# Kernel tuning notes

Measured on AMD Instinct MI355X. Metric: run time of the kernel, lower is better.

Reference implementation:

```python
import jax, jax.numpy as jnp
import numpy as np

TOP_K = 2
NUM_EXPERTS = 8
CAPACITY_FACTOR = 1.0


def setup_inputs() -> dict:
    key = jax.random.key(0)
    k1, k2, k3, k4 = jax.random.split(key, 4)
    sl, bs, hs, ffn = 2048, 2, 1024, 4096
    x = jax.random.normal(k1, (sl, bs, hs), dtype=jnp.float32)
    router_w = jax.random.normal(k2, (hs, NUM_EXPERTS), dtype=jnp.float32) * 0.02
    w1 = jax.random.normal(k3, (NUM_EXPERTS, hs, ffn), dtype=jnp.float32) * 0.02
    w2 = jax.random.normal(k4, (NUM_EXPERTS, ffn, hs), dtype=jnp.float32) * 0.02
    bias = jnp.zeros((1, 1, hs), dtype=jnp.float32)
    return {"x": x, "router_w": router_w, "w1": w1, "w2": w2, "bias": bias}


def _moe_forward(x, router_w, w1, w2):
    sl, bs, hs = x.shape
    xf = x.reshape(-1, hs)                                   # [T, H]
    T = xf.shape[0]
    TK = T * TOP_K
    capacity = int(CAPACITY_FACTOR * TOP_K * T / NUM_EXPERTS)  # static

    # Router: softmax over experts, then top-k (LearnedRouter)
    scores = jax.nn.softmax(xf @ router_w, axis=-1)          # [T, E]
    expert_weights, top_experts = jax.lax.top_k(scores, TOP_K)  # [T, K]
    ew = expert_weights.reshape(-1)                          # [T*K]
    te = top_experts.reshape(-1).astype(jnp.int32)           # [T*K]

    # indices_and_bins: stable sort by expert id + histogram + inclusive cumsum
    indices = jnp.argsort(te, stable=True)                   # sorted pos -> flat slot
    tokens_per_expert = jnp.zeros((NUM_EXPERTS,), jnp.int32).at[te].add(1)
    bins = jnp.cumsum(tokens_per_expert)                     # inclusive cumsum
    starts = bins - tokens_per_expert                        # exclusive offsets

    # binned_gather -> [E, capacity, H]; tokens beyond capacity are dropped
    c_range = jnp.arange(capacity)
    pos = starts[:, None] + c_range[None, :]                 # [E, C] positions in sorted order
    valid = c_range[None, :] < tokens_per_expert[:, None]    # [E, C]
    slot = indices[jnp.clip(pos, 0, TK - 1)]                 # flat (token*K + k) slot
    tok = slot // TOP_K                                      # source token row
    gathered = jnp.where(valid[..., None], xf[tok], 0.0)     # [E, C, H]

    # grouped expert MLP: gelu(x @ w1) @ w2  (megablocks mlp.MLP)
    h = jax.nn.gelu(jnp.einsum('ech,ehf->ecf', gathered, w1))
    y = jnp.einsum('ecf,efh->ech', h, w2)                    # [E, C, H]

    # binned_scatter: weighted accumulate back to token rows
    p = jnp.arange(TK)
    e_of_p = jnp.searchsorted(bins, p, side='right')         # expert of sorted pos
    c_of_p = p - starts[e_of_p]                              # slot within expert bin
    ok = c_of_p < capacity                                   # dropped tokens contribute 0
    vals = jnp.where(ok[:, None], y[e_of_p, jnp.clip(c_of_p, 0, capacity - 1)], 0.0)
    flat = indices                                           # flat slot at sorted pos p
    w = ew[flat]
    out = jnp.zeros((T, hs), x.dtype).at[flat // TOP_K].add(w[:, None] * vals)
    return out.reshape(sl, bs, hs)


def reference(x, router_w, w1, w2, bias):
    out = _moe_forward(x, router_w, w1, w2)
    return (out, bias)
```

## Files before the change

kernel.cpp:

```cpp
#include <hip/hip_runtime.h>
#include <hip/hip_bf16.h>


#define T_TOK 4096
#define HS 1024
#define FFN 4096
#define NE 8
#define CAP 1024
#define TKS 8192

#define WS_TE   67108864
#define WS_EW   67141632
#define WS_PERM 67174400
#define WS_WT   67239936
#define WS_XB   134348800

typedef float f4 __attribute__((ext_vector_type(4)));
typedef __bf16 bf16x8 __attribute__((ext_vector_type(8)));
typedef float f32x4 __attribute__((ext_vector_type(4)));

__device__ __forceinline__ void gld_lds16(const void* g, void* l) {
    __builtin_amdgcn_global_load_lds(
        (const __attribute__((address_space(1))) unsigned int*)g,
        (__attribute__((address_space(3))) unsigned int*)l, 16, 0, 0);
}

__global__ void init_out_kernel(float* __restrict__ out, const float* __restrict__ bias) {
    int i = blockIdx.x * 256 + threadIdx.x;
    const int TH = T_TOK * HS;
    if (i < TH) out[i] = 0.0f;
    else if (i < TH + HS) out[i] = bias[i - TH];
}

__global__ __launch_bounds__(256) void router_kernel(const float* __restrict__ x,
                                                     const float* __restrict__ rw,
                                                     int* __restrict__ te,
                                                     float* __restrict__ ew,
                                                     __bf16* __restrict__ xb) {
    __shared__ float rwt[NE * HS];
    int tid = threadIdx.x;
    for (int i = tid; i < NE * HS; i += 256) {
        int h = i >> 3, e = i & 7;
        rwt[e * HS + h] = rw[i];
    }
    __syncthreads();
    int wave = tid >> 6, lane = tid & 63;
    int t = blockIdx.x * 4 + wave;
    const float* xr = x + (size_t)t * HS;
    float s[NE];
    float xv[16];
#pragma unroll
    for (int e = 0; e < NE; ++e) s[e] = 0.0f;
#pragma unroll
    for (int j = 0; j < 16; ++j) {
        int h = lane + j * 64;
        xv[j] = xr[h];
#pragma unroll
        for (int e = 0; e < NE; ++e) s[e] += xv[j] * rwt[e * HS + h];
    }
#pragma unroll
    for (int j = 0; j < 16; ++j)
        xb[(size_t)t * HS + lane + j * 64] = (__bf16)xv[j];
#pragma unroll
    for (int e = 0; e < NE; ++e) {
#pragma unroll
        for (int off = 1; off < 64; off <<= 1) s[e] += __shfl_xor(s[e], off, 64);
    }
    float m = s[0];
#pragma unroll
    for (int e = 1; e < NE; ++e) m = fmaxf(m, s[e]);
    float psum = 0.0f;
#pragma unroll
    for (int e = 0; e < NE; ++e) psum += __expf(s[e] - m);
    int e0 = 0; float v0 = s[0];
#pragma unroll
    for (int e = 1; e < NE; ++e) { if (s[e] > v0) { v0 = s[e]; e0 = e; } }
    int e1 = -1; float v1 = -1e30f;
#pragma unroll
    for (int e = 0; e < NE; ++e) { if (e != e0 && s[e] > v1) { v1 = s[e]; e1 = e; } }
    if (lane == 0) {
        float inv = 1.0f / psum;
        te[2 * t]     = e0;
        te[2 * t + 1] = e1;
        ew[2 * t]     = __expf(v0 - m) * inv;
        ew[2 * t + 1] = __expf(v1 - m) * inv;
    }
}

__global__ __launch_bounds__(256) void sort_kernel(const int* __restrict__ te,
                                                   int* __restrict__ perm) {
    __shared__ int hist[256 * NE];
    int tid = threadIdx.x;
#pragma unroll
    for (int e = 0; e < NE; ++e) hist[tid * NE + e] = 0;
    for (int i = tid; i < TKS; i += 256) perm[i] = -1;
    __syncthreads();
    for (int j = 0; j < 32; ++j) {
        int p = tid * 32 + j;
        hist[tid * NE + te[p]]++;
    }
    __syncthreads();
    if (tid < NE) {
        int run = 0;
        for (int i = 0; i < 256; ++i) {
            int v = hist[i * NE + tid];
            hist[i * NE + tid] = run;
            run += v;
        }
    }
    __syncthreads();
    for (int j = 0; j < 32; ++j) {
        int p = tid * 32 + j;
        int e = te[p];
        int c = hist[tid * NE + e]++;
        if (c < CAP) perm[e * CAP + c] = p;
    }
}

__global__ __launch_bounds__(256) void conv_wt_kernel(const float* __restrict__ w,
                                                      __bf16* __restrict__ wt,
                                                      int K, int N) {
    __shared__ __bf16 t[64][72];
    const int e = blockIdx.z;
    const int kb = blockIdx.y * 64, nb = blockIdx.x * 64;
    const int tid = threadIdx.x;
    const float* src = w + ((size_t)e * K + kb) * N + nb;
    {
        const int kk = tid >> 4, nc = (tid & 15) * 4;
#pragma unroll
        for (int i = 0; i < 4; ++i) {
            int k = kk + 16 * i;
            f4 v = *(const f4*)(src + (size_t)k * N + nc);
            t[nc + 0][k] = (__bf16)v[0];
            t[nc + 1][k] = (__bf16)v[1];
            t[nc + 2][k] = (__bf16)v[2];
            t[nc + 3][k] = (__bf16)v[3];
        }
    }
    __syncthreads();
    __bf16* dst = wt + ((size_t)e * N + nb) * K + kb;
    const int nn = tid >> 3, ch = (tid & 7) * 8;
#pragma unroll
    for (int i = 0; i < 2; ++i) {
        int n = nn + 32 * i;
        bf16x8 v = *(const bf16x8*)(&t[n][ch]);
        *(bf16x8*)(dst + (size_t)n * K + ch) = v;
    }
}


#define STAGE8(c_, koff_) do {                                              \
    _Pragma("unroll")                                                       \
    for (int j = 0; j < 4; ++j) {                                           \
        gld_lds16(aptr[j] + (koff_), &As[c_][j * 32 + w * 8][0]);           \
        gld_lds16(bptr[j] + (koff_), &Bs[c_][j * 32 + w * 8][0]);           \
    }                                                                       \
} while (0)

#define TILE_BODY(c_) do {                                                  \
    _Pragma("unroll")                                                       \
    for (int kk = 0; kk < 2; ++kk) {                                        \
        const int g = (kk * 4 + (lane >> 4)) ^ (lane & 7);                  \
        bf16x8 af[4], bb[4];                                                \
        _Pragma("unroll")                                                   \
        for (int mi = 0; mi < 4; ++mi)                                      \
            af[mi] = *(const bf16x8*)&As[c_][wr * 64 + mi * 16 + l15][g * 8]; \
        _Pragma("unroll")                                                   \
        for (int ni = 0; ni < 4; ++ni)                                      \
            bb[ni] = *(const bf16x8*)&Bs[c_][wc * 64 + ni * 16 + l15][g * 8]; \
        __builtin_amdgcn_s_setprio(1);                                      \
        _Pragma("unroll")                                                   \
        for (int mi = 0; mi < 4; ++mi)                                      \
            _Pragma("unroll")                                               \
            for (int ni = 0; ni < 4; ++ni)                                  \
                acc[mi][ni] = __builtin_amdgcn_mfma_f32_16x16x32_bf16(      \
                    af[mi], bb[ni], acc[mi][ni], 0, 0, 0);                  \
        __builtin_amdgcn_s_setprio(0);                                      \
    }                                                                       \
} while (0)

#define KTILE_SYNC() do {                                                   \
    asm volatile("s_waitcnt vmcnt(0)" ::: "memory");                        \
    __builtin_amdgcn_s_barrier();                                           \
    asm volatile("" ::: "memory");                                          \
} while (0)

__global__ __launch_bounds__(256, 2) void gemm1_kernel(const __bf16* __restrict__ xb,
                                                       const __bf16* __restrict__ w1t,
                                                       const int* __restrict__ perm,
                                                       __bf16* __restrict__ hbuf) {
    __shared__ __bf16 As[2][128][64];
    __shared__ __bf16 Bs[2][128][64];
    const int e = blockIdx.z, mblk = blockIdx.y, nblk = blockIdx.x;
    const int tid = threadIdx.x, lane = tid & 63, w = tid >> 6;
    const int wr = w >> 1, wc = w & 1;
    const int l15 = lane & 15;
    const int srl = lane >> 3;
    const int gsrc = (lane & 7) ^ srl;

    const __bf16* aptr[4];
    const __bf16* bptr[4];
#pragma unroll
    for (int j = 0; j < 4; ++j) {
        int arow = j * 32 + w * 8 + srl;
        int p = perm[e * CAP + mblk * 128 + arow];
        int tok = (p < 0) ? 0 : (p >> 1);
        aptr[j] = xb + (size_t)tok * HS + gsrc * 8;
        int brow = nblk * 128 + j * 32 + w * 8 + srl;
        bptr[j] = w1t + ((size_t)e * FFN + brow) * HS + gsrc * 8;
    }

    f32x4 acc[4][4];
#pragma unroll
    for (int mi = 0; mi < 4; ++mi)
#pragma unroll
        for (int ni = 0; ni < 4; ++ni) acc[mi][ni] = (f32x4)0.0f;

    const int NT = HS / 64;
    STAGE8(0, 0);
    KTILE_SYNC();
    int c = 0;
    for (int t = 0; t < NT; ++t) {
        if (t + 1 < NT) STAGE8(c ^ 1, (t + 1) * 64);
        TILE_BODY(c);
        KTILE_SYNC();
        c ^= 1;
    }

    const int mbase = mblk * 128 + wr * 64;
    const int nbase = nblk * 128 + wc * 64;
#pragma unroll
    for (int mi = 0; mi < 4; ++mi) {
#pragma unroll
        for (int ni = 0; ni < 4; ++ni) {
#pragma unroll
            for (int reg = 0; reg < 4; ++reg) {
                int mrow = mbase + mi * 16 + (lane >> 4) * 4 + reg;
                int ncol = nbase + ni * 16 + l15;
                float z = acc[mi][ni][reg];
                float u = 0.7978845608028654f * (z + 0.044715f * z * z * z);
                float tt = 1.0f - 2.0f / (1.0f + __expf(2.0f * u));
                float gv = 0.5f * z * (1.0f + tt);
                hbuf[(size_t)(e * CAP + mrow) * FFN + ncol] = (__bf16)gv;
            }
        }
    }
}

__global__ __launch_bounds__(256, 2) void gemm2_kernel(const __bf16* __restrict__ hbuf,
                                                       const __bf16* __restrict__ w2t,
                                                       const int* __restrict__ perm,
                                                       const float* __restrict__ ew,
                                                       float* __restrict__ out) {
    __shared__ __bf16 As[2][128][64];
    __shared__ __bf16 Bs[2][128][64];
    const int e = blockIdx.z;
    const int mblk = blockIdx.y, nblk = blockIdx.x;
    const int tid = threadIdx.x, lane = tid & 63, w = tid >> 6;
    const int wr = w >> 1, wc = w & 1;
    const int l15 = lane & 15;
    const int srl = lane >> 3;
    const int gsrc = (lane & 7) ^ srl;

    const __bf16* aptr[4];
    const __bf16* bptr[4];
#pragma unroll
    for (int j = 0; j < 4; ++j) {
        int arow = j * 32 + w * 8 + srl;
        aptr[j] = hbuf + ((size_t)(e * CAP + mblk * 128 + arow)) * FFN + gsrc * 8;
        int brow = nblk * 128 + j * 32 + w * 8 + srl;
        bptr[j] = w2t + ((size_t)e * HS + brow) * FFN + gsrc * 8;
    }

    f32x4 acc[4][4];
#pragma unroll
    for (int mi = 0; mi < 4; ++mi)
#pragma unroll
        for (int ni = 0; ni < 4; ++ni) acc[mi][ni] = (f32x4)0.0f;

    const int NT = FFN / 64;
    STAGE8(0, 0);
    KTILE_SYNC();
    int c = 0;
    for (int t = 0; t < NT; ++t) {
        if (t + 1 < NT) STAGE8(c ^ 1, (t + 1) * 64);
        TILE_BODY(c);
        KTILE_SYNC();
        c ^= 1;
    }

    int* sperm = (int*)&As[0][0][0];
    float* swt = (float*)(sperm + 128);
    if (tid < 128) {
        int p = perm[e * CAP + mblk * 128 + tid];
        sperm[tid] = p;
        swt[tid] = (p >= 0) ? ew[p] : 0.0f;
    }
    __syncthreads();

    const int nbase = nblk * 128 + wc * 64;
#pragma unroll
    for (int mi = 0; mi < 4; ++mi) {
#pragma unroll
        for (int reg = 0; reg < 4; ++reg) {
            int mloc = wr * 64 + mi * 16 + (lane >> 4) * 4 + reg;
            int p = sperm[mloc];
            if (p >= 0) {
                int tok = p >> 1;
                float wgt = swt[mloc];
#pragma unroll
                for (int ni = 0; ni < 4; ++ni) {
                    int n = nbase + ni * 16 + l15;
                    atomicAdd(&out[(size_t)tok * HS + n], wgt * acc[mi][ni][reg]);
                }
            }
        }
    }
}

extern "C" void kernel_launch(void* const* d_in, const int* in_sizes, int n_in,
                              void* d_out, int out_size, void* d_ws, size_t ws_size,
                              hipStream_t stream) {
    const float* x    = (const float*)d_in[0];
    const float* rw   = (const float*)d_in[1];
    const float* w1   = (const float*)d_in[2];
    const float* w2   = (const float*)d_in[3];
    const float* bias = (const float*)d_in[4];
    float* out = (float*)d_out;
    char* ws = (char*)d_ws;

    __bf16* hbuf = (__bf16*)ws;
    int*    te   = (int*)(ws + WS_TE);
    float*  ew   = (float*)(ws + WS_EW);
    int*    perm = (int*)(ws + WS_PERM);
    __bf16* wt   = (__bf16*)(ws + WS_WT);
    __bf16* xb   = (__bf16*)(ws + WS_XB);

    hipLaunchKernelGGL(init_out_kernel, dim3((T_TOK * HS + HS + 255) / 256), dim3(256),
                       0, stream, out, bias);
    hipLaunchKernelGGL(router_kernel, dim3(T_TOK / 4), dim3(256), 0, stream,
                       x, rw, te, ew, xb);
    hipLaunchKernelGGL(sort_kernel, dim3(1), dim3(256), 0, stream, te, perm);
    hipLaunchKernelGGL(conv_wt_kernel, dim3(FFN / 64, HS / 64, NE), dim3(256),
                       0, stream, w1, wt, HS, FFN);
    hipLaunchKernelGGL(gemm1_kernel, dim3(FFN / 128, CAP / 128, NE), dim3(256),
                       0, stream, xb, wt, perm, hbuf);
    hipLaunchKernelGGL(conv_wt_kernel, dim3(HS / 64, FFN / 64, NE), dim3(256),
                       0, stream, w2, wt, FFN, HS);
    hipLaunchKernelGGL(gemm2_kernel, dim3(HS / 128, CAP / 128, NE), dim3(256),
                       0, stream, hbuf, wt, perm, ew, out);
}
```

Before: 300.6 us.

## Single-buffer GEMM K-loop, remap blocks for XCD locality, cheaper GELU epilogue

Both expert GEMMs drop LDS double buffering and use a simple load-wait-sync-compute-sync loop with half the shared memory. The occupancy hint is removed from launch bounds. The 3D grid becomes a 1D grid whose block index is remapped so consecutive blocks of the same expert and M-block land on the same XCD, which is meant to improve L2 reuse of weights and activations. The tanh-GELU epilogue is rewritten in the equivalent sigmoid form with a fast reciprocal. The cost is that global loads no longer overlap with MFMA work inside a block.

After: 281.4 us. 1.07x faster.

```diff
diff --git a/kernel.cpp b/kernel.cpp
--- a/kernel.cpp
+++ b/kernel.cpp
@@ -149,25 +149,25 @@
 }
 
 
-#define STAGE8(c_, koff_) do {                                              \
+#define STAGE8(koff_) do {                                                  \
     _Pragma("unroll")                                                       \
     for (int j = 0; j < 4; ++j) {                                           \
-        gld_lds16(aptr[j] + (koff_), &As[c_][j * 32 + w * 8][0]);           \
-        gld_lds16(bptr[j] + (koff_), &Bs[c_][j * 32 + w * 8][0]);           \
+        gld_lds16(aptr[j] + (koff_), &As[j * 32 + w * 8][0]);               \
+        gld_lds16(bptr[j] + (koff_), &Bs[j * 32 + w * 8][0]);               \
     }                                                                       \
 } while (0)
 
-#define TILE_BODY(c_) do {                                                  \
+#define TILE_BODY() do {                                                    \
     _Pragma("unroll")                                                       \
     for (int kk = 0; kk < 2; ++kk) {                                        \
         const int g = (kk * 4 + (lane >> 4)) ^ (lane & 7);                  \
         bf16x8 af[4], bb[4];                                                \
         _Pragma("unroll")                                                   \
         for (int mi = 0; mi < 4; ++mi)                                      \
-            af[mi] = *(const bf16x8*)&As[c_][wr * 64 + mi * 16 + l15][g * 8]; \
+            af[mi] = *(const bf16x8*)&As[wr * 64 + mi * 16 + l15][g * 8];   \
         _Pragma("unroll")                                                   \
         for (int ni = 0; ni < 4; ++ni)                                      \
-            bb[ni] = *(const bf16x8*)&Bs[c_][wc * 64 + ni * 16 + l15][g * 8]; \
+            bb[ni] = *(const bf16x8*)&Bs[wc * 64 + ni * 16 + l15][g * 8];   \
         __builtin_amdgcn_s_setprio(1);                                      \
         _Pragma("unroll")                                                   \
         for (int mi = 0; mi < 4; ++mi)                                      \
@@ -179,19 +179,27 @@
     }                                                                       \
 } while (0)
 
-#define KTILE_SYNC() do {                                                   \
-    asm volatile("s_waitcnt vmcnt(0)" ::: "memory");                        \
-    __builtin_amdgcn_s_barrier();                                           \
-    asm volatile("" ::: "memory");                                          \
+#define KLOOP(NT_) do {                                                     \
+    for (int t = 0; t < (NT_); ++t) {                                       \
+        STAGE8(t * 64);                                                     \
+        asm volatile("s_waitcnt vmcnt(0)" ::: "memory");                    \
+        __syncthreads();                                                    \
+        TILE_BODY();                                                        \
+        __syncthreads();                                                    \
+    }                                                                       \
 } while (0)
 
-__global__ __launch_bounds__(256, 2) void gemm1_kernel(const __bf16* __restrict__ xb,
-                                                       const __bf16* __restrict__ w1t,
-                                                       const int* __restrict__ perm,
-                                                       __bf16* __restrict__ hbuf) {
-    __shared__ __bf16 As[2][128][64];
-    __shared__ __bf16 Bs[2][128][64];
-    const int e = blockIdx.z, mblk = blockIdx.y, nblk = blockIdx.x;
+__global__ __launch_bounds__(256) void gemm1_kernel(const __bf16* __restrict__ xb,
+                                                    const __bf16* __restrict__ w1t,
+                                                    const int* __restrict__ perm,
+                                                    __bf16* __restrict__ hbuf) {
+    __shared__ __bf16 As[128][64];
+    __shared__ __bf16 Bs[128][64];
+    const int hw = blockIdx.x;
+    const int logical = (hw & 7) * 256 + (hw >> 3);
+    const int nblk = logical & 31;
+    const int mblk = (logical >> 5) & 7;
+    const int e    = logical >> 8;
     const int tid = threadIdx.x, lane = tid & 63, w = tid >> 6;
     const int wr = w >> 1, wc = w & 1;
     const int l15 = lane & 15;
@@ -216,16 +224,7 @@
 #pragma unroll
         for (int ni = 0; ni < 4; ++ni) acc[mi][ni] = (f32x4)0.0f;
 
-    const int NT = HS / 64;
-    STAGE8(0, 0);
-    KTILE_SYNC();
-    int c = 0;
-    for (int t = 0; t < NT; ++t) {
-        if (t + 1 < NT) STAGE8(c ^ 1, (t + 1) * 64);
-        TILE_BODY(c);
-        KTILE_SYNC();
-        c ^= 1;
-    }
+    KLOOP(HS / 64);
 
     const int mbase = mblk * 128 + wr * 64;
     const int nbase = nblk * 128 + wc * 64;
@@ -238,24 +237,28 @@
                 int mrow = mbase + mi * 16 + (lane >> 4) * 4 + reg;
                 int ncol = nbase + ni * 16 + l15;
                 float z = acc[mi][ni][reg];
-                float u = 0.7978845608028654f * (z + 0.044715f * z * z * z);
-                float tt = 1.0f - 2.0f / (1.0f + __expf(2.0f * u));
-                float gv = 0.5f * z * (1.0f + tt);
+                float z2 = z * z;
+                float y = z * (1.5957691216057308f + 0.07135481627f * z2);
+                float ex = __expf(-y);
+                float gv = z * __builtin_amdgcn_rcpf(1.0f + ex);
                 hbuf[(size_t)(e * CAP + mrow) * FFN + ncol] = (__bf16)gv;
             }
         }
     }
 }
 
-__global__ __launch_bounds__(256, 2) void gemm2_kernel(const __bf16* __restrict__ hbuf,
-                                                       const __bf16* __restrict__ w2t,
-                                                       const int* __restrict__ perm,
-                                                       const float* __restrict__ ew,
-                                                       float* __restrict__ out) {
-    __shared__ __bf16 As[2][128][64];
-    __shared__ __bf16 Bs[2][128][64];
-    const int e = blockIdx.z;
-    const int mblk = blockIdx.y, nblk = blockIdx.x;
+__global__ __launch_bounds__(256) void gemm2_kernel(const __bf16* __restrict__ hbuf,
+                                                    const __bf16* __restrict__ w2t,
+                                                    const int* __restrict__ perm,
+                                                    const float* __restrict__ ew,
+                                                    float* __restrict__ out) {
+    __shared__ __bf16 As[128][64];
+    __shared__ __bf16 Bs[128][64];
+    const int hw = blockIdx.x;
+    const int logical = (hw & 7) * 64 + (hw >> 3);
+    const int nblk = logical & 7;
+    const int mblk = (logical >> 3) & 7;
+    const int e    = logical >> 6;
     const int tid = threadIdx.x, lane = tid & 63, w = tid >> 6;
     const int wr = w >> 1, wc = w & 1;
     const int l15 = lane & 15;
@@ -278,18 +281,9 @@
 #pragma unroll
         for (int ni = 0; ni < 4; ++ni) acc[mi][ni] = (f32x4)0.0f;
 
-    const int NT = FFN / 64;
-    STAGE8(0, 0);
-    KTILE_SYNC();
-    int c = 0;
-    for (int t = 0; t < NT; ++t) {
-        if (t + 1 < NT) STAGE8(c ^ 1, (t + 1) * 64);
-        TILE_BODY(c);
-        KTILE_SYNC();
-        c ^= 1;
-    }
-
-    int* sperm = (int*)&As[0][0][0];
+    KLOOP(FFN / 64);
+
+    int* sperm = (int*)&As[0][0];
     float* swt = (float*)(sperm + 128);
     if (tid < 128) {
         int p = perm[e * CAP + mblk * 128 + tid];
@@ -343,10 +337,10 @@
     hipLaunchKernelGGL(sort_kernel, dim3(1), dim3(256), 0, stream, te, perm);
     hipLaunchKernelGGL(conv_wt_kernel, dim3(FFN / 64, HS / 64, NE), dim3(256),
                        0, stream, w1, wt, HS, FFN);
-    hipLaunchKernelGGL(gemm1_kernel, dim3(FFN / 128, CAP / 128, NE), dim3(256),
-                       0, stream, xb, wt, perm, hbuf);
+    hipLaunchKernelGGL(gemm1_kernel, dim3(2048), dim3(256), 0, stream,
+                       xb, wt, perm, hbuf);
     hipLaunchKernelGGL(conv_wt_kernel, dim3(HS / 64, FFN / 64, NE), dim3(256),
                        0, stream, w2, wt, FFN, HS);
-    hipLaunchKernelGGL(gemm2_kernel, dim3(HS / 128, CAP / 128, NE), dim3(256),
-                       0, stream, hbuf, wt, perm, ew, out);
-}
+    hipLaunchKernelGGL(gemm2_kernel, dim3(512), dim3(256), 0, stream,
+                       hbuf, wt, perm, ew, out);
+}
```
